# Kernel optimization log

Measured on AMD Instinct MI355X. Metric: run time of the kernel, lower is better.

The kernel has to match this reference:

```python
import jax, jax.numpy as jnp
import numpy as np

N_NODES = 10000  # static number of graph nodes (segment count)


def setup_inputs() -> dict:
    key = jax.random.key(0)
    ks = jax.random.split(key, 7)
    B, N, DIN, DOUT, E = 2, N_NODES, 256, 256, 320000
    x = jax.random.normal(ks[0], (B, N, DIN), dtype=jnp.float32)
    W = jax.random.normal(ks[1], (DIN, DOUT), dtype=jnp.float32) * (1.0 / np.sqrt(DIN))
    loop_W = jax.random.normal(ks[2], (DIN, DOUT), dtype=jnp.float32) * (1.0 / np.sqrt(DIN))
    bias = jax.random.normal(ks[3], (DOUT,), dtype=jnp.float32) * 0.01
    edge_vals = jax.random.uniform(ks[4], (E,), dtype=jnp.float32)
    rows = jax.random.randint(ks[5], (E,), 0, N, dtype=jnp.int32)
    cols = jax.random.randint(ks[6], (E,), 0, N, dtype=jnp.int32)
    return {"x": x, "W": W, "loop_W": loop_W, "bias": bias,
            "edge_vals": edge_vals, "rows": rows, "cols": cols}


def reference(x, W, loop_W, bias, edge_vals, rows, cols):
    # Dense feature transforms: [b,n,din] @ [din,dout] -> [b,n,dout]
    support = jnp.einsum('bni,io->bno', x, W)
    support_loop = jnp.einsum('bni,io->bno', x, loop_W)
    # Sparse adjacency matmul (COO SpMM): out[r] += val_e * support[:, c_e, :]
    msgs = support[:, cols, :] * edge_vals[None, :, None]      # [b, E, dout]
    agg = jax.ops.segment_sum(
        jnp.swapaxes(msgs, 0, 1), rows, num_segments=N_NODES)   # [n, b, dout]
    agg = jnp.swapaxes(agg, 0, 1)                                # [b, n, dout]
    out = agg + support_loop + bias
    return jax.nn.relu(out)
```

## Files before the change

kernel.cpp:

```cpp
#include <hip/hip_runtime.h>
#include <hip/hip_bf16.h>


#define NN 10000
#define DK 256
#define DO 256
#define MT 20000
#define SCAN_T 1024
#define SCAN_C 10

typedef short short8 __attribute__((ext_vector_type(8)));
typedef float f32x4 __attribute__((ext_vector_type(4)));

__device__ inline unsigned short f2bf(float f) {
    unsigned int u = __float_as_uint(f);
    u = (u + 0x7FFFu + ((u >> 16) & 1u)) >> 16;
    return (unsigned short)u;
}
__device__ inline float bf2f(unsigned short s) {
    return __uint_as_float(((unsigned int)s) << 16);
}

__global__ __launch_bounds__(256) void prep_kernel(
    const float* __restrict__ W, const float* __restrict__ LW,
    unsigned short* __restrict__ Wt, unsigned short* __restrict__ LWt,
    const int* __restrict__ rows, int* __restrict__ counts, int E)
{
    __shared__ float tile[64][65];
    const int bid = blockIdx.x;
    if (bid < 32) {
        const int z = bid >> 4, rem = bid & 15;
        const int k0 = (rem >> 2) * 64, c0 = (rem & 3) * 64;
        const float* src = z ? LW : W;
        unsigned short* dst = z ? LWt : Wt;
        #pragma unroll
        for (int it = 0; it < 16; ++it) {
            const int u = it * 256 + threadIdx.x;
            const int i = u >> 6, j = u & 63;
            tile[i][j] = src[(size_t)(k0 + i) * DO + c0 + j];
        }
        __syncthreads();
        #pragma unroll
        for (int it = 0; it < 16; ++it) {
            const int u = it * 256 + threadIdx.x;
            const int j = u >> 6, i = u & 63;
            dst[(size_t)(c0 + j) * DK + k0 + i] = f2bf(tile[i][j]);
        }
    } else {
        const int e = (bid - 32) * 256 + threadIdx.x;
        if (e < E) atomicAdd(&counts[rows[e]], 1);
    }
}

__global__ __launch_bounds__(SCAN_T) void scan_rows(
    const int* __restrict__ counts, int* __restrict__ offsets,
    int* __restrict__ cursor)
{
    __shared__ int sums[SCAN_T];
    const int t = threadIdx.x;
    int local[SCAN_C];
    int s = 0;
    const int base = t * SCAN_C;
    #pragma unroll
    for (int i = 0; i < SCAN_C; ++i) {
        const int idx = base + i;
        const int c = (idx < NN) ? counts[idx] : 0;
        local[i] = s;
        s += c;
    }
    sums[t] = s;
    __syncthreads();
    for (int off = 1; off < SCAN_T; off <<= 1) {
        int u = (t >= off) ? sums[t - off] : 0;
        __syncthreads();
        sums[t] += u;
        __syncthreads();
    }
    const int excl = (t == 0) ? 0 : sums[t - 1];
    #pragma unroll
    for (int i = 0; i < SCAN_C; ++i) {
        const int idx = base + i;
        if (idx < NN) {
            const int o = excl + local[i];
            offsets[idx] = o;
            cursor[idx]  = o;
        }
    }
}

__global__ __launch_bounds__(256) void main_kernel(
    const float* __restrict__ X, const unsigned short* __restrict__ Wt,
    const unsigned short* __restrict__ LWt, const float* __restrict__ bias,
    unsigned short* __restrict__ sup, float* __restrict__ outv,
    const int* __restrict__ rows, const int* __restrict__ cols,
    const float* __restrict__ vals, int* __restrict__ cursor,
    float2* __restrict__ epack, int E, int gemmBlocks)
{
    __shared__ unsigned short As[8][64][8];
    __shared__ unsigned short BsW[8][64][8];
    __shared__ unsigned short BsL[8][64][8];

    if (blockIdx.x >= gemmBlocks) {
        const int e = (blockIdx.x - gemmBlocks) * 256 + threadIdx.x;
        if (e < E) {
            const int p = atomicAdd(&cursor[rows[e]], 1);
            epack[p] = make_float2(__int_as_float(cols[e]), vals[e]);
        }
        return;
    }

    const int t = threadIdx.x;
    const int wid = t >> 6, lane = t & 63;
    const int wm = wid >> 1, wn = wid & 1;
    const int m0 = (blockIdx.x >> 2) * 64;
    const int n0 = (blockIdx.x & 3) * 64;

    f32x4 accW[2][2], accL[2][2];
    #pragma unroll
    for (int i = 0; i < 2; ++i)
        #pragma unroll
        for (int j = 0; j < 2; ++j) {
            accW[i][j] = (f32x4){0.f, 0.f, 0.f, 0.f};
            accL[i][j] = (f32x4){0.f, 0.f, 0.f, 0.f};
        }

    for (int k0 = 0; k0 < DK; k0 += 64) {
        #pragma unroll
        for (int it = 0; it < 2; ++it) {
            const int u = it * 256 + t;
            const int row = u >> 3, kg = u & 7;
            const int grow = m0 + row;
            short8 v = (short8){0,0,0,0,0,0,0,0};
            if (grow < MT) {
                const float4 a = *(const float4*)&X[(size_t)grow * DK + k0 + kg * 8];
                const float4 b = *(const float4*)&X[(size_t)grow * DK + k0 + kg * 8 + 4];
                v[0] = (short)f2bf(a.x); v[1] = (short)f2bf(a.y);
                v[2] = (short)f2bf(a.z); v[3] = (short)f2bf(a.w);
                v[4] = (short)f2bf(b.x); v[5] = (short)f2bf(b.y);
                v[6] = (short)f2bf(b.z); v[7] = (short)f2bf(b.w);
            }
            *(short8*)&As[kg][row ^ kg][0] = v;
        }
        #pragma unroll
        for (int it = 0; it < 2; ++it) {
            const int u = it * 256 + t;
            const int col = u >> 3, kg = u & 7;
            const size_t off = (size_t)(n0 + col) * DK + k0 + kg * 8;
            *(short8*)&BsW[kg][col ^ kg][0] = *(const short8*)&Wt[off];
            *(short8*)&BsL[kg][col ^ kg][0] = *(const short8*)&LWt[off];
        }
        __syncthreads();
        #pragma unroll
        for (int s = 0; s < 2; ++s) {
            const int kg = s * 4 + (lane >> 4);
            short8 af[2], bW[2], bL[2];
            #pragma unroll
            for (int i = 0; i < 2; ++i) {
                const int row = wm * 32 + i * 16 + (lane & 15);
                af[i] = *(const short8*)&As[kg][row ^ kg][0];
            }
            #pragma unroll
            for (int j = 0; j < 2; ++j) {
                const int col = wn * 32 + j * 16 + (lane & 15);
                bW[j] = *(const short8*)&BsW[kg][col ^ kg][0];
                bL[j] = *(const short8*)&BsL[kg][col ^ kg][0];
            }
            #pragma unroll
            for (int i = 0; i < 2; ++i)
                #pragma unroll
                for (int j = 0; j < 2; ++j) {
                    accW[i][j] = __builtin_amdgcn_mfma_f32_16x16x32_bf16(
                        af[i], bW[j], accW[i][j], 0, 0, 0);
                    accL[i][j] = __builtin_amdgcn_mfma_f32_16x16x32_bf16(
                        af[i], bL[j], accL[i][j], 0, 0, 0);
                }
        }
        __syncthreads();
    }

    const int rbase = m0 + wm * 32;
    const int cbase = n0 + wn * 32;
    #pragma unroll
    for (int i = 0; i < 2; ++i)
        #pragma unroll
        for (int q = 0; q < 4; ++q) {
            const int row = rbase + i * 16 + (lane >> 4) * 4 + q;
            if (row < MT) {
                #pragma unroll
                for (int j = 0; j < 2; ++j) {
                    const int col = cbase + j * 16 + (lane & 15);
                    sup[(size_t)row * DO + col] = f2bf(accW[i][j][q]);
                    outv[(size_t)row * DO + col] = accL[i][j][q] + bias[col];
                }
            }
        }
}

__global__ __launch_bounds__(256) void agg_relu(
    const unsigned short* __restrict__ sup, const float2* __restrict__ epack,
    const int* __restrict__ offsets, const int* __restrict__ counts,
    float* __restrict__ outv)
{
    const int widx = (blockIdx.x * 256 + threadIdx.x) >> 6;
    if (widx >= 2 * NN) return;
    const int lane = threadIdx.x & 63;
    const int b = widx & 1, r = widx >> 1;
    const int d = lane * 4;
    const size_t supb = (size_t)b * NN * DO + d;
    const int start = offsets[r];
    const int deg   = counts[r];

    float a0 = 0.f, a1 = 0.f, a2 = 0.f, a3 = 0.f;
    #pragma unroll 8
    for (int i = 0; i < deg; ++i) {
        const float2 ep = epack[start + i];
        const int col = __float_as_int(ep.x);
        const float v = ep.y;
        const ushort4 s = *(const ushort4*)&sup[supb + (size_t)col * DO];
        a0 += v * bf2f(s.x); a1 += v * bf2f(s.y);
        a2 += v * bf2f(s.z); a3 += v * bf2f(s.w);
    }

    float* o = &outv[((size_t)b * NN + r) * DO + d];
    float4 t4 = *(const float4*)o;
    t4.x = fmaxf(t4.x + a0, 0.f); t4.y = fmaxf(t4.y + a1, 0.f);
    t4.z = fmaxf(t4.z + a2, 0.f); t4.w = fmaxf(t4.w + a3, 0.f);
    *(float4*)o = t4;
}

extern "C" void kernel_launch(void* const* d_in, const int* in_sizes, int n_in,
                              void* d_out, int out_size, void* d_ws, size_t ws_size,
                              hipStream_t stream)
{
    const float* x    = (const float*)d_in[0];
    const float* W    = (const float*)d_in[1];
    const float* LW   = (const float*)d_in[2];
    const float* bias = (const float*)d_in[3];
    const float* ev   = (const float*)d_in[4];
    const int*   rows = (const int*)d_in[5];
    const int*   cols = (const int*)d_in[6];
    float* out = (float*)d_out;

    const int E = in_sizes[4];
    const int EB = (E + 255) / 256;
    const int gemmBlocks = ((MT + 63) / 64) * 4;

    char* wsb = (char*)d_ws;
    unsigned short* Wt    = (unsigned short*)wsb;
    unsigned short* LWt   = (unsigned short*)(wsb + 131072);
    unsigned short* supb  = (unsigned short*)(wsb + 262144);
    int* counts  = (int*)(wsb + 10502144);
    int* offsets = (int*)(wsb + 10542144);
    int* cursor  = (int*)(wsb + 10582144);
    float2* epack = (float2*)(wsb + 10622144);

    hipMemsetAsync(counts, 0, NN * sizeof(int), stream);

    prep_kernel<<<32 + EB, 256, 0, stream>>>(W, LW, Wt, LWt, rows, counts, E);
    scan_rows<<<1, SCAN_T, 0, stream>>>(counts, offsets, cursor);
    main_kernel<<<gemmBlocks + EB, 256, 0, stream>>>(
        x, Wt, LWt, bias, supb, out, rows, cols, ev, cursor, epack, E, gemmBlocks);

    const int aggBlocks = (2 * NN * 64 + 255) / 256;
    agg_relu<<<aggBlocks, 256, 0, stream>>>(supb, epack, offsets, counts, out);
}
```

Baseline: 121.1 us.

## Pipeline GEMM column quarters with aggregation of previous quarter across launches

```diff
diff --git a/kernel.cpp b/kernel.cpp
--- a/kernel.cpp
+++ b/kernel.cpp
@@ -8,6 +8,8 @@
 #define MT 20000
 #define SCAN_T 1024
 #define SCAN_C 10
+#define GQ 313
+#define AGB 1250
 
 typedef short short8 __attribute__((ext_vector_type(8)));
 typedef float f32x4 __attribute__((ext_vector_type(4)));
@@ -88,32 +90,65 @@
     }
 }
 
-__global__ __launch_bounds__(256) void main_kernel(
+__global__ __launch_bounds__(256) void stage_kernel(
     const float* __restrict__ X, const unsigned short* __restrict__ Wt,
     const unsigned short* __restrict__ LWt, const float* __restrict__ bias,
     unsigned short* __restrict__ sup, float* __restrict__ outv,
     const int* __restrict__ rows, const int* __restrict__ cols,
     const float* __restrict__ vals, int* __restrict__ cursor,
-    float2* __restrict__ epack, int E, int gemmBlocks)
+    float2* __restrict__ epack, const int* __restrict__ offsets,
+    const int* __restrict__ counts, int E,
+    int nGemm, int nq, int fq, int extraMode)
 {
     __shared__ unsigned short As[8][64][8];
     __shared__ unsigned short BsW[8][64][8];
     __shared__ unsigned short BsL[8][64][8];
 
-    if (blockIdx.x >= gemmBlocks) {
-        const int e = (blockIdx.x - gemmBlocks) * 256 + threadIdx.x;
-        if (e < E) {
-            const int p = atomicAdd(&cursor[rows[e]], 1);
-            epack[p] = make_float2(__int_as_float(cols[e]), vals[e]);
-        }
+    if ((int)blockIdx.x >= nGemm) {
+        const int ebid = blockIdx.x - nGemm;
+        if (extraMode == 0) {
+            const int e = ebid * 256 + threadIdx.x;
+            if (e < E) {
+                const int p = atomicAdd(&cursor[rows[e]], 1);
+                epack[p] = make_float2(__int_as_float(cols[e]), vals[e]);
+            }
+            return;
+        }
+        const int wid = threadIdx.x >> 6, lane = threadIdx.x & 63;
+        const int widx = ebid * 4 + wid;
+        if (widx >= NN / 2) return;
+        const int sub = lane >> 4;
+        const int rsel = sub >> 1, b = sub & 1;
+        const int r = widx * 2 + rsel;
+        const int f0 = fq * 64 + (lane & 15) * 4;
+        const int start = offsets[r];
+        const int deg   = counts[r];
+        const size_t supb = (size_t)b * NN * DO + f0;
+
+        float a0 = 0.f, a1 = 0.f, a2 = 0.f, a3 = 0.f;
+        #pragma unroll 8
+        for (int i = 0; i < deg; ++i) {
+            const float2 ep = epack[start + i];
+            const int col = __float_as_int(ep.x);
+            const float v = ep.y;
+            const ushort4 s = *(const ushort4*)&sup[supb + (size_t)col * DO];
+            a0 += v * bf2f(s.x); a1 += v * bf2f(s.y);
+            a2 += v * bf2f(s.z); a3 += v * bf2f(s.w);
+        }
+
+        float* o = &outv[((size_t)b * NN + r) * DO + f0];
+        float4 t4 = *(const float4*)o;
+        t4.x = fmaxf(t4.x + a0, 0.f); t4.y = fmaxf(t4.y + a1, 0.f);
+        t4.z = fmaxf(t4.z + a2, 0.f); t4.w = fmaxf(t4.w + a3, 0.f);
+        *(float4*)o = t4;
         return;
     }
 
     const int t = threadIdx.x;
     const int wid = t >> 6, lane = t & 63;
     const int wm = wid >> 1, wn = wid & 1;
-    const int m0 = (blockIdx.x >> 2) * 64;
-    const int n0 = (blockIdx.x & 3) * 64;
+    const int m0 = blockIdx.x * 64;
+    const int n0 = nq * 64;
 
     f32x4 accW[2][2], accL[2][2];
     #pragma unroll
@@ -141,13 +176,14 @@
             }
             *(short8*)&As[kg][row ^ kg][0] = v;
         }
-        #pragma unroll
-        for (int it = 0; it < 2; ++it) {
-            const int u = it * 256 + t;
-            const int col = u >> 3, kg = u & 7;
-            const size_t off = (size_t)(n0 + col) * DK + k0 + kg * 8;
-            *(short8*)&BsW[kg][col ^ kg][0] = *(const short8*)&Wt[off];
-            *(short8*)&BsL[kg][col ^ kg][0] = *(const short8*)&LWt[off];
+        {
+            const int u = t;
+            const int col = u >> 2, kg2 = (u & 3) * 2;
+            const size_t off = (size_t)(n0 + col) * DK + k0 + kg2 * 8;
+            *(short8*)&BsW[kg2][col ^ kg2][0]           = *(const short8*)&Wt[off];
+            *(short8*)&BsW[kg2 + 1][col ^ (kg2 + 1)][0] = *(const short8*)&Wt[off + 8];
+            *(short8*)&BsL[kg2][col ^ kg2][0]           = *(const short8*)&LWt[off];
+            *(short8*)&BsL[kg2 + 1][col ^ (kg2 + 1)][0] = *(const short8*)&LWt[off + 8];
         }
         __syncthreads();
         #pragma unroll
@@ -196,38 +232,6 @@
         }
 }
 
-__global__ __launch_bounds__(256) void agg_relu(
-    const unsigned short* __restrict__ sup, const float2* __restrict__ epack,
-    const int* __restrict__ offsets, const int* __restrict__ counts,
-    float* __restrict__ outv)
-{
-    const int widx = (blockIdx.x * 256 + threadIdx.x) >> 6;
-    if (widx >= 2 * NN) return;
-    const int lane = threadIdx.x & 63;
-    const int b = widx & 1, r = widx >> 1;
-    const int d = lane * 4;
-    const size_t supb = (size_t)b * NN * DO + d;
-    const int start = offsets[r];
-    const int deg   = counts[r];
-
-    float a0 = 0.f, a1 = 0.f, a2 = 0.f, a3 = 0.f;
-    #pragma unroll 8
-    for (int i = 0; i < deg; ++i) {
-        const float2 ep = epack[start + i];
-        const int col = __float_as_int(ep.x);
-        const float v = ep.y;
-        const ushort4 s = *(const ushort4*)&sup[supb + (size_t)col * DO];
-        a0 += v * bf2f(s.x); a1 += v * bf2f(s.y);
-        a2 += v * bf2f(s.z); a3 += v * bf2f(s.w);
-    }
-
-    float* o = &outv[((size_t)b * NN + r) * DO + d];
-    float4 t4 = *(const float4*)o;
-    t4.x = fmaxf(t4.x + a0, 0.f); t4.y = fmaxf(t4.y + a1, 0.f);
-    t4.z = fmaxf(t4.z + a2, 0.f); t4.w = fmaxf(t4.w + a3, 0.f);
-    *(float4*)o = t4;
-}
-
 extern "C" void kernel_launch(void* const* d_in, const int* in_sizes, int n_in,
                               void* d_out, int out_size, void* d_ws, size_t ws_size,
                               hipStream_t stream)
@@ -243,7 +247,6 @@
 
     const int E = in_sizes[4];
     const int EB = (E + 255) / 256;
-    const int gemmBlocks = ((MT + 63) / 64) * 4;
 
     char* wsb = (char*)d_ws;
     unsigned short* Wt    = (unsigned short*)wsb;
@@ -258,9 +261,13 @@
 
     prep_kernel<<<32 + EB, 256, 0, stream>>>(W, LW, Wt, LWt, rows, counts, E);
     scan_rows<<<1, SCAN_T, 0, stream>>>(counts, offsets, cursor);
-    main_kernel<<<gemmBlocks + EB, 256, 0, stream>>>(
-        x, Wt, LWt, bias, supb, out, rows, cols, ev, cursor, epack, E, gemmBlocks);
-
-    const int aggBlocks = (2 * NN * 64 + 255) / 256;
-    agg_relu<<<aggBlocks, 256, 0, stream>>>(supb, epack, offsets, counts, out);
-}
+
+    #define STAGE_ARGS x, Wt, LWt, bias, supb, out, rows, cols, ev, cursor, \
+                       epack, offsets, counts, E
+    stage_kernel<<<GQ + EB, 256, 0, stream>>>(STAGE_ARGS, GQ, 0, -1, 0);
+    stage_kernel<<<GQ + AGB, 256, 0, stream>>>(STAGE_ARGS, GQ, 1, 0, 1);
+    stage_kernel<<<GQ + AGB, 256, 0, stream>>>(STAGE_ARGS, GQ, 2, 1, 1);
+    stage_kernel<<<GQ + AGB, 256, 0, stream>>>(STAGE_ARGS, GQ, 3, 2, 1);
+    stage_kernel<<<AGB, 256, 0, stream>>>(STAGE_ARGS, 0, -1, 3, 1);
+    #undef STAGE_ARGS
+}
```

Result: slower. 151.2 us (+24.9%).

## Register-prefetch GEMM tiles and split aggregation into feature-quarter passes

Applied to the files above, without the earlier changes.

```diff
diff --git a/kernel.cpp b/kernel.cpp
--- a/kernel.cpp
+++ b/kernel.cpp
@@ -100,7 +100,7 @@
     __shared__ unsigned short BsW[8][64][8];
     __shared__ unsigned short BsL[8][64][8];
 
-    if (blockIdx.x >= gemmBlocks) {
+    if ((int)blockIdx.x >= gemmBlocks) {
         const int e = (blockIdx.x - gemmBlocks) * 256 + threadIdx.x;
         if (e < E) {
             const int p = atomicAdd(&cursor[rows[e]], 1);
@@ -115,6 +115,9 @@
     const int m0 = (blockIdx.x >> 2) * 64;
     const int n0 = (blockIdx.x & 3) * 64;
 
+    const int srow0 = t >> 3, skg0 = t & 7;
+    const int srow1 = (256 + t) >> 3, skg1 = t & 7;
+
     f32x4 accW[2][2], accL[2][2];
     #pragma unroll
     for (int i = 0; i < 2; ++i)
@@ -124,32 +127,47 @@
             accL[i][j] = (f32x4){0.f, 0.f, 0.f, 0.f};
         }
 
-    for (int k0 = 0; k0 < DK; k0 += 64) {
-        #pragma unroll
-        for (int it = 0; it < 2; ++it) {
-            const int u = it * 256 + t;
-            const int row = u >> 3, kg = u & 7;
-            const int grow = m0 + row;
-            short8 v = (short8){0,0,0,0,0,0,0,0};
-            if (grow < MT) {
-                const float4 a = *(const float4*)&X[(size_t)grow * DK + k0 + kg * 8];
-                const float4 b = *(const float4*)&X[(size_t)grow * DK + k0 + kg * 8 + 4];
-                v[0] = (short)f2bf(a.x); v[1] = (short)f2bf(a.y);
-                v[2] = (short)f2bf(a.z); v[3] = (short)f2bf(a.w);
-                v[4] = (short)f2bf(b.x); v[5] = (short)f2bf(b.y);
-                v[6] = (short)f2bf(b.z); v[7] = (short)f2bf(b.w);
-            }
-            *(short8*)&As[kg][row ^ kg][0] = v;
-        }
-        #pragma unroll
-        for (int it = 0; it < 2; ++it) {
-            const int u = it * 256 + t;
-            const int col = u >> 3, kg = u & 7;
-            const size_t off = (size_t)(n0 + col) * DK + k0 + kg * 8;
-            *(short8*)&BsW[kg][col ^ kg][0] = *(const short8*)&Wt[off];
-            *(short8*)&BsL[kg][col ^ kg][0] = *(const short8*)&LWt[off];
-        }
-        __syncthreads();
+    float4 pa[2][2];
+    short8 pbW[2], pbL[2];
+
+    #define LOAD_TILE(K0)                                                        \
+    {                                                                            \
+        const int rows_[2] = {srow0, srow1};                                     \
+        _Pragma("unroll")                                                        \
+        for (int it = 0; it < 2; ++it) {                                         \
+            const int grow = m0 + rows_[it];                                     \
+            if (grow < MT) {                                                     \
+                pa[it][0] = *(const float4*)&X[(size_t)grow * DK + (K0) + skg0 * 8];     \
+                pa[it][1] = *(const float4*)&X[(size_t)grow * DK + (K0) + skg0 * 8 + 4]; \
+            } else {                                                             \
+                pa[it][0] = make_float4(0.f, 0.f, 0.f, 0.f);                     \
+                pa[it][1] = make_float4(0.f, 0.f, 0.f, 0.f);                     \
+            }                                                                    \
+            const size_t boff = (size_t)(n0 + rows_[it]) * DK + (K0) + skg0 * 8; \
+            pbW[it] = *(const short8*)&Wt[boff];                                 \
+            pbL[it] = *(const short8*)&LWt[boff];                                \
+        }                                                                        \
+    }
+
+    LOAD_TILE(0);
+
+    for (int k = 0; k < 4; ++k) {
+        {
+            const int rows_[2] = {srow0, srow1};
+            #pragma unroll
+            for (int it = 0; it < 2; ++it) {
+                short8 v;
+                v[0] = (short)f2bf(pa[it][0].x); v[1] = (short)f2bf(pa[it][0].y);
+                v[2] = (short)f2bf(pa[it][0].z); v[3] = (short)f2bf(pa[it][0].w);
+                v[4] = (short)f2bf(pa[it][1].x); v[5] = (short)f2bf(pa[it][1].y);
+                v[6] = (short)f2bf(pa[it][1].z); v[7] = (short)f2bf(pa[it][1].w);
+                *(short8*)&As[skg0][rows_[it] ^ skg0][0] = v;
+                *(short8*)&BsW[skg0][rows_[it] ^ skg0][0] = pbW[it];
+                *(short8*)&BsL[skg0][rows_[it] ^ skg0][0] = pbL[it];
+            }
+        }
+        __syncthreads();
+        if (k < 3) LOAD_TILE((k + 1) * 64);
         #pragma unroll
         for (int s = 0; s < 2; ++s) {
             const int kg = s * 4 + (lane >> 4);
@@ -177,6 +195,7 @@
         }
         __syncthreads();
     }
+    #undef LOAD_TILE
 
     const int rbase = m0 + wm * 32;
     const int cbase = n0 + wn * 32;
@@ -196,19 +215,21 @@
         }
 }
 
-__global__ __launch_bounds__(256) void agg_relu(
+__global__ __launch_bounds__(256) void agg_q(
     const unsigned short* __restrict__ sup, const float2* __restrict__ epack,
     const int* __restrict__ offsets, const int* __restrict__ counts,
-    float* __restrict__ outv)
+    float* __restrict__ outv, int fq)
 {
     const int widx = (blockIdx.x * 256 + threadIdx.x) >> 6;
-    if (widx >= 2 * NN) return;
+    if (widx >= NN / 2) return;
     const int lane = threadIdx.x & 63;
-    const int b = widx & 1, r = widx >> 1;
-    const int d = lane * 4;
-    const size_t supb = (size_t)b * NN * DO + d;
+    const int sub = lane >> 4;
+    const int rsel = sub >> 1, b = sub & 1;
+    const int r = widx * 2 + rsel;
+    const int f0 = fq * 64 + (lane & 15) * 4;
     const int start = offsets[r];
     const int deg   = counts[r];
+    const size_t supb = (size_t)b * NN * DO + f0;
 
     float a0 = 0.f, a1 = 0.f, a2 = 0.f, a3 = 0.f;
     #pragma unroll 8
@@ -221,7 +242,7 @@
         a2 += v * bf2f(s.z); a3 += v * bf2f(s.w);
     }
 
-    float* o = &outv[((size_t)b * NN + r) * DO + d];
+    float* o = &outv[((size_t)b * NN + r) * DO + f0];
     float4 t4 = *(const float4*)o;
     t4.x = fmaxf(t4.x + a0, 0.f); t4.y = fmaxf(t4.y + a1, 0.f);
     t4.z = fmaxf(t4.z + a2, 0.f); t4.w = fmaxf(t4.w + a3, 0.f);
@@ -261,6 +282,7 @@
     main_kernel<<<gemmBlocks + EB, 256, 0, stream>>>(
         x, Wt, LWt, bias, supb, out, rows, cols, ev, cursor, epack, E, gemmBlocks);
 
-    const int aggBlocks = (2 * NN * 64 + 255) / 256;
-    agg_relu<<<aggBlocks, 256, 0, stream>>>(supb, epack, offsets, counts, out);
-}
+    const int aggBlocks = (NN / 2 * 64 + 255) / 256;
+    for (int fq = 0; fq < 4; ++fq)
+        agg_q<<<aggBlocks, 256, 0, stream>>>(supb, epack, offsets, counts, out, fq);
+}
```

Result: slower. 133.8 us (+10.5%).

## Pre-convert X to bf16 and stage GEMM tiles with direct global-to-LDS loads

Applied to the files above, without the earlier changes.

```diff
diff --git a/kernel.cpp b/kernel.cpp
--- a/kernel.cpp
+++ b/kernel.cpp
@@ -8,9 +8,14 @@
 #define MT 20000
 #define SCAN_T 1024
 #define SCAN_C 10
+#define CVB 2500
 
 typedef short short8 __attribute__((ext_vector_type(8)));
 typedef float f32x4 __attribute__((ext_vector_type(4)));
+
+#define GLOAD_LDS(G, L) __builtin_amdgcn_global_load_lds(                 \
+    (const __attribute__((address_space(1))) void*)(G),                   \
+    (__attribute__((address_space(3))) void*)(L), 16, 0, 0)
 
 __device__ inline unsigned short f2bf(float f) {
     unsigned int u = __float_as_uint(f);
@@ -22,14 +27,26 @@
 }
 
 __global__ __launch_bounds__(256) void prep_kernel(
+    const float* __restrict__ X, unsigned short* __restrict__ Xb,
     const float* __restrict__ W, const float* __restrict__ LW,
     unsigned short* __restrict__ Wt, unsigned short* __restrict__ LWt,
     const int* __restrict__ rows, int* __restrict__ counts, int E)
 {
     __shared__ float tile[64][65];
     const int bid = blockIdx.x;
-    if (bid < 32) {
-        const int z = bid >> 4, rem = bid & 15;
+    if (bid < CVB) {
+        const int i = bid * 256 + threadIdx.x;
+        const float4 a = ((const float4*)X)[2 * i];
+        const float4 b = ((const float4*)X)[2 * i + 1];
+        short8 o;
+        o[0] = (short)f2bf(a.x); o[1] = (short)f2bf(a.y);
+        o[2] = (short)f2bf(a.z); o[3] = (short)f2bf(a.w);
+        o[4] = (short)f2bf(b.x); o[5] = (short)f2bf(b.y);
+        o[6] = (short)f2bf(b.z); o[7] = (short)f2bf(b.w);
+        *(short8*)&Xb[(size_t)i * 8] = o;
+    } else if (bid < CVB + 32) {
+        const int zb = bid - CVB;
+        const int z = zb >> 4, rem = zb & 15;
         const int k0 = (rem >> 2) * 64, c0 = (rem & 3) * 64;
         const float* src = z ? LW : W;
         unsigned short* dst = z ? LWt : Wt;
@@ -47,7 +64,7 @@
             dst[(size_t)(c0 + j) * DK + k0 + i] = f2bf(tile[i][j]);
         }
     } else {
-        const int e = (bid - 32) * 256 + threadIdx.x;
+        const int e = (bid - CVB - 32) * 256 + threadIdx.x;
         if (e < E) atomicAdd(&counts[rows[e]], 1);
     }
 }
@@ -89,18 +106,18 @@
 }
 
 __global__ __launch_bounds__(256) void main_kernel(
-    const float* __restrict__ X, const unsigned short* __restrict__ Wt,
+    const unsigned short* __restrict__ Xb, const unsigned short* __restrict__ Wt,
     const unsigned short* __restrict__ LWt, const float* __restrict__ bias,
     unsigned short* __restrict__ sup, float* __restrict__ outv,
     const int* __restrict__ rows, const int* __restrict__ cols,
     const float* __restrict__ vals, int* __restrict__ cursor,
     float2* __restrict__ epack, int E, int gemmBlocks)
 {
-    __shared__ unsigned short As[8][64][8];
-    __shared__ unsigned short BsW[8][64][8];
-    __shared__ unsigned short BsL[8][64][8];
-
-    if (blockIdx.x >= gemmBlocks) {
+    __shared__ unsigned short Abuf[8 * 64 * 8];
+    __shared__ unsigned short BbufW[8 * 64 * 8];
+    __shared__ unsigned short BbufL[8 * 64 * 8];
+
+    if ((int)blockIdx.x >= gemmBlocks) {
         const int e = (blockIdx.x - gemmBlocks) * 256 + threadIdx.x;
         if (e < E) {
             const int p = atomicAdd(&cursor[rows[e]], 1);
@@ -126,28 +143,15 @@
 
     for (int k0 = 0; k0 < DK; k0 += 64) {
         #pragma unroll
-        for (int it = 0; it < 2; ++it) {
-            const int u = it * 256 + t;
-            const int row = u >> 3, kg = u & 7;
-            const int grow = m0 + row;
-            short8 v = (short8){0,0,0,0,0,0,0,0};
-            if (grow < MT) {
-                const float4 a = *(const float4*)&X[(size_t)grow * DK + k0 + kg * 8];
-                const float4 b = *(const float4*)&X[(size_t)grow * DK + k0 + kg * 8 + 4];
-                v[0] = (short)f2bf(a.x); v[1] = (short)f2bf(a.y);
-                v[2] = (short)f2bf(a.z); v[3] = (short)f2bf(a.w);
-                v[4] = (short)f2bf(b.x); v[5] = (short)f2bf(b.y);
-                v[6] = (short)f2bf(b.z); v[7] = (short)f2bf(b.w);
-            }
-            *(short8*)&As[kg][row ^ kg][0] = v;
-        }
-        #pragma unroll
-        for (int it = 0; it < 2; ++it) {
-            const int u = it * 256 + t;
-            const int col = u >> 3, kg = u & 7;
-            const size_t off = (size_t)(n0 + col) * DK + k0 + kg * 8;
-            *(short8*)&BsW[kg][col ^ kg][0] = *(const short8*)&Wt[off];
-            *(short8*)&BsL[kg][col ^ kg][0] = *(const short8*)&LWt[off];
+        for (int c = 0; c < 2; ++c) {
+            const int kg = c * 4 + wid;
+            const int src_r = lane ^ kg;
+            const size_t aoff = (size_t)(m0 + src_r) * DK + k0 + kg * 8;
+            const size_t boff = (size_t)(n0 + src_r) * DK + k0 + kg * 8;
+            unsigned short* ldst = &Abuf[(c * 256 + wid * 64) * 8];
+            GLOAD_LDS(&Xb[aoff], ldst);
+            GLOAD_LDS(&Wt[boff],  &BbufW[(c * 256 + wid * 64) * 8]);
+            GLOAD_LDS(&LWt[boff], &BbufL[(c * 256 + wid * 64) * 8]);
         }
         __syncthreads();
         #pragma unroll
@@ -157,13 +161,13 @@
             #pragma unroll
             for (int i = 0; i < 2; ++i) {
                 const int row = wm * 32 + i * 16 + (lane & 15);
-                af[i] = *(const short8*)&As[kg][row ^ kg][0];
+                af[i] = *(const short8*)&Abuf[((size_t)kg * 64 + (row ^ kg)) * 8];
             }
             #pragma unroll
             for (int j = 0; j < 2; ++j) {
                 const int col = wn * 32 + j * 16 + (lane & 15);
-                bW[j] = *(const short8*)&BsW[kg][col ^ kg][0];
-                bL[j] = *(const short8*)&BsL[kg][col ^ kg][0];
+                bW[j] = *(const short8*)&BbufW[((size_t)kg * 64 + (col ^ kg)) * 8];
+                bL[j] = *(const short8*)&BbufL[((size_t)kg * 64 + (col ^ kg)) * 8];
             }
             #pragma unroll
             for (int i = 0; i < 2; ++i)
@@ -248,18 +252,20 @@
     char* wsb = (char*)d_ws;
     unsigned short* Wt    = (unsigned short*)wsb;
     unsigned short* LWt   = (unsigned short*)(wsb + 131072);
-    unsigned short* supb  = (unsigned short*)(wsb + 262144);
-    int* counts  = (int*)(wsb + 10502144);
-    int* offsets = (int*)(wsb + 10542144);
-    int* cursor  = (int*)(wsb + 10582144);
-    float2* epack = (float2*)(wsb + 10622144);
+    unsigned short* Xb    = (unsigned short*)(wsb + 262144);
+    unsigned short* supb  = (unsigned short*)(wsb + 10518528);
+    int* counts  = (int*)(wsb + 20758528);
+    int* offsets = (int*)(wsb + 20798528);
+    int* cursor  = (int*)(wsb + 20838528);
+    float2* epack = (float2*)(wsb + 20878528);
 
     hipMemsetAsync(counts, 0, NN * sizeof(int), stream);
 
-    prep_kernel<<<32 + EB, 256, 0, stream>>>(W, LW, Wt, LWt, rows, counts, E);
+    prep_kernel<<<CVB + 32 + EB, 256, 0, stream>>>(
+        x, Xb, W, LW, Wt, LWt, rows, counts, E);
     scan_rows<<<1, SCAN_T, 0, stream>>>(counts, offsets, cursor);
     main_kernel<<<gemmBlocks + EB, 256, 0, stream>>>(
-        x, Wt, LWt, bias, supb, out, rows, cols, ev, cursor, epack, E, gemmBlocks);
+        Xb, Wt, LWt, bias, supb, out, rows, cols, ev, cursor, epack, E, gemmBlocks);
 
     const int aggBlocks = (2 * NN * 64 + 255) / 256;
     agg_relu<<<aggBlocks, 256, 0, stream>>>(supb, epack, offsets, counts, out);
```

After: 123.6 us. +2.1%, slower.
